# Optimization experiments

Hardware: AMD Instinct MI355X
Metric: run time of the kernel (lower is better)

## Reference

```python
import jax, jax.numpy as jnp
import numpy as np
from jax import lax

B, H, W, C = 8, 128, 128, 256
HEADS, DHEAD = 8, 32
INNER = HEADS * DHEAD  # == C, required by pos_emb reshape


def setup_inputs() -> dict:
    key = jax.random.key(0)
    ks = jax.random.split(key, 12)
    s = 0.02
    return {
        "x_in": jax.random.normal(ks[0], (B, H, W, C), jnp.float32),
        "Wq": jax.random.normal(ks[1], (INNER, C), jnp.float32) * s,
        "Wk": jax.random.normal(ks[2], (INNER, C), jnp.float32) * s,
        "Wv": jax.random.normal(ks[3], (INNER, C), jnp.float32) * s,
        "rescale": jnp.ones((HEADS, 1, 1), jnp.float32),
        "Wp": jax.random.normal(ks[4], (C, INNER), jnp.float32) * s,
        "bp": jnp.zeros((C,), jnp.float32),
        "Wc1": jax.random.normal(ks[5], (INNER, INNER, 3, 3), jnp.float32) * s,
        "bc1": jnp.zeros((INNER,), jnp.float32),
        "Wc2": jax.random.normal(ks[6], (INNER, INNER, 3, 3), jnp.float32) * s,
        "bc2": jnp.zeros((INNER,), jnp.float32),
    }


def _l2norm(x, axis=-1, eps=1e-12):
    n = jnp.sqrt(jnp.sum(x * x, axis=axis, keepdims=True))
    return x / jnp.maximum(n, eps)


def _conv(x, w, b):
    y = lax.conv_general_dilated(x, w, (1, 1), 'SAME',
                                 dimension_numbers=('NCHW', 'OIHW', 'NCHW'))
    return y + b[None, :, None, None]


def reference(x_in, Wq, Wk, Wv, rescale, Wp, bp, Wc1, bc1, Wc2, bc2):
    b, h, w, c = x_in.shape
    n = h * w
    x = x_in.reshape(b, n, c)
    q_inp = x @ Wq.T  # [b, n, inner]
    k_inp = x @ Wk.T
    v_inp = x @ Wv.T

    def heads(t):  # b n (h d) -> b h d n  (already transposed)
        return t.reshape(b, n, HEADS, DHEAD).transpose(0, 2, 3, 1)

    q = _l2norm(heads(q_inp))  # [b, heads, d, n], normalized over n
    k = _l2norm(heads(k_inp))
    v = heads(v_inp)  # [b, heads, d, n]

    attn = jnp.einsum('bhdn,bhen->bhde', k, q) * rescale  # [b, heads, d, d]
    attn = jax.nn.softmax(attn, axis=-1)
    xo = jnp.einsum('bhde,bhen->bhdn', attn, v)  # [b, heads, d, n]
    xo = xo.transpose(0, 3, 1, 2).reshape(b, n, INNER)  # b n (heads d)
    out_c = (xo @ Wp.T + bp).reshape(b, h, w, c)

    vp = v_inp.reshape(b, h, w, INNER).transpose(0, 3, 1, 2)  # NCHW
    p = _conv(vp, Wc1, bc1)
    p = jax.nn.gelu(p, approximate=False)
    p = _conv(p, Wc2, bc2)
    out_p = p.transpose(0, 2, 3, 1)  # b h w c
    return out_c, out_p
```

## Files before the change

### kernel.cpp

```cpp
#include <hip/hip_runtime.h>
#include <cstdint>

#define DEV __device__ __forceinline__

typedef __bf16 bf16x8 __attribute__((ext_vector_type(8)));
typedef float f32x4 __attribute__((ext_vector_type(4)));
typedef unsigned int u32;
typedef unsigned short u16;

DEV u16 f2bf(float f) {
  u32 u = __builtin_bit_cast(u32, f);
  u += 0x7fffu + ((u >> 16) & 1u);
  return (u16)(u >> 16);
}
DEV float bf2f(u16 b) { return __builtin_bit_cast(float, (u32)b << 16); }

DEV void gload16(const u16* g, u16* l) {
  __builtin_amdgcn_global_load_lds(
      (const __attribute__((address_space(1))) u32*)g,
      (__attribute__((address_space(3))) u32*)(uintptr_t)l, 16, 0, 0);
}

DEV void border_body(u16* __restrict__ p, int idx) {
  int pix = idx >> 5, c8 = (idx & 31) << 3;
  int b = pix / 516, r = pix % 516;
  int x, y;
  if (r < 130)      { y = 0;   x = r; }
  else if (r < 260) { y = 129; x = r - 130; }
  else if (r < 388) { x = 0;   y = r - 259; }
  else              { x = 129; y = r - 387; }
  u16* dst = p + (((long)b * 130 + y) * 130 + x) * 256 + c8;
  *reinterpret_cast<uint4*>(dst) = uint4{0, 0, 0, 0};
}

__global__ void cvt_f32_bf16(const float* __restrict__ in, u16* __restrict__ out, int n4) {
  int i = blockIdx.x * blockDim.x + threadIdx.x;
  if (i >= n4) return;
  float4 v = reinterpret_cast<const float4*>(in)[i];
  ushort4 o;
  o.x = f2bf(v.x); o.y = f2bf(v.y); o.z = f2bf(v.z); o.w = f2bf(v.w);
  reinterpret_cast<ushort4*>(out)[i] = o;
}

__global__ void prep(const float* __restrict__ Wq, const float* __restrict__ Wk,
                     const float* __restrict__ Wv, const float* __restrict__ Wc1,
                     const float* __restrict__ Wc2, u16* __restrict__ wqkv,
                     u16* __restrict__ wc1r, u16* __restrict__ wc2r, u16* __restrict__ vpad) {
  const int blk = blockIdx.x, t = threadIdx.x;
  if (blk < 192) {
    const float* src = blk < 64 ? Wq : (blk < 128 ? Wk : Wv);
    u16* dst = wqkv + (blk < 64 ? 0 : (blk < 128 ? 65536 : 131072));
    const int i = (blk & 63) * 256 + t;
    float4 v = reinterpret_cast<const float4*>(src)[i];
    ushort4 o;
    o.x = f2bf(v.x); o.y = f2bf(v.y); o.z = f2bf(v.z); o.w = f2bf(v.w);
    reinterpret_cast<ushort4*>(dst)[i] = o;
  } else if (blk < 4800) {
    const int q = blk - 192;
    const float* w = q < 2304 ? Wc1 : Wc2;
    u16* dst = q < 2304 ? wc1r : wc2r;
    const int j = (q % 2304) * 256 + t;
    const int oc = j / 2304, r = j - oc * 2304;
    const int kt = r >> 6, c_lo = r & 63;
    const int cg = kt / 9, slab = kt - cg * 9;
    const int ic = cg * 64 + c_lo;
    dst[j] = f2bf(w[(oc * 256 + ic) * 9 + slab]);
  } else {
    const int idx = (blk - 4800) * 256 + t;
    if (idx < 8 * 516 * 32) border_body(vpad, idx);
  }
}

template <int CONV, int KTOT, int EPI, int PERB, int SWZ>
__global__ __launch_bounds__(512, 1) void mm8(
    const u16* __restrict__ A, const u16* __restrict__ Bt,
    const float* __restrict__ bias, void* __restrict__ out,
    u16* __restrict__ vp) {
  extern __shared__ u16 lds[];
  constexpr int NKT = KTOT / 64;
  constexpr int NITER = NKT / 2;
  const int tid = threadIdx.x;
  const int wave = tid >> 6, lane = tid & 63;
  const int wr = wave >> 2, wcid = wave & 3;
  const int lrow = lane & 15, lk = lane >> 4;
  int bid = (int)blockIdx.x;
  int tile, colbase;
  if (SWZ == 1) {
    const int xcd = bid & 7, k = bid >> 3;
    tile = (xcd + ((k >> 5) << 3)) * 32 + (k & 31);
    colbase = 0;
  } else if (SWZ == 2) {
    const int xcd = bid & 7, s = bid >> 3;
    const int r = s / 3;
    tile = xcd * 64 + r;
    colbase = (s - r * 3) * 256;
  } else {
    tile = (bid & 7) * 64 + (bid >> 3);
    colbase = 0;
  }
  const long rowbase = (long)tile * 256;
  const int bimg = tile >> 6;
  const int y0 = (tile & 63) * 2;
  const u16* BT = PERB ? Bt + (long)bimg * 65536 : Bt;

  auto STAGE = [&](int kt, int isB, int half, int bufq) {
#pragma unroll
    for (int j = 0; j < 2; ++j) {
      const int idx = j * 512 + tid;
      const int rh = idx >> 3;
      const int sg = (idx & 7) ^ (rh & 7);
      const u16* g;
      if (isB) {
        g = BT + (long)(colbase + half * 128 + rh) * KTOT + kt * 64 + sg * 8;
      } else if (CONV == 1) {
        const int cg = kt / 9;
        const int slab = kt - cg * 9;
        const int ky = slab / 3 - 1, kx = slab - (slab / 3) * 3 - 1;
        const int c0 = cg * 64;
        g = A + (((long)bimg * 130 + (y0 + half) + 1 + ky) * 130 + (rh + 1 + kx)) * 256 + c0 + sg * 8;
      } else if (CONV == 2) {
        g = A + (((long)bimg * 130 + (y0 + half) + 1) * 130 + (rh + 1)) * 256 + kt * 64 + sg * 8;
      } else {
        g = A + (rowbase + half * 128 + rh) * (long)256 + kt * 64 + sg * 8;
      }
      u16* l = lds + (isB ? 32768 : 0) + bufq * 16384 + half * 8192 + (j * 512 + wave * 64) * 8;
      gload16(g, l);
    }
  };

  f32x4 acc[8][4] = {};
  bf16x8 bq[4][2];

  STAGE(0, 1, 0, 0); STAGE(0, 1, 1, 0);
  STAGE(0, 0, 0, 0); STAGE(0, 0, 1, 0);
  STAGE(1, 1, 0, 1); STAGE(1, 1, 1, 1);
  asm volatile("s_waitcnt vmcnt(4)" ::: "memory");
  __builtin_amdgcn_s_barrier();
  __builtin_amdgcn_sched_barrier(0);

  for (int it = 0; it < NITER; ++it) {
    const int u0 = 2 * it;
#pragma unroll
    for (int ph = 0; ph < 8; ++ph) {
      constexpr int S_ISB[8]  = {0, 0, 1, 1, 0, 0, 1, 1};
      constexpr int S_HALF[8] = {0, 1, 0, 1, 0, 1, 0, 1};
      constexpr int S_BUF[8]  = {1, 1, 0, 0, 0, 0, 1, 1};
      constexpr int S_DT[8]   = {1, 1, 2, 2, 2, 2, 3, 3};
      const int cbuf = ph >> 2, quad = ph & 3;
      if (quad == 0) {
#pragma unroll
        for (int nf = 0; nf < 4; ++nf)
#pragma unroll
          for (int ks = 0; ks < 2; ++ks) {
            const int n = wcid * 64 + nf * 16 + lrow;
            const int slot = (ks * 4 + lk) ^ (n & 7);
            bq[nf][ks] = *reinterpret_cast<const bf16x8*>(&lds[32768 + cbuf * 16384 + n * 64 + slot * 8]);
          }
      }
      bf16x8 aq[2][2];
#pragma unroll
      for (int mf = 0; mf < 2; ++mf)
#pragma unroll
        for (int ks = 0; ks < 2; ++ks) {
          const int r = wr * 128 + quad * 32 + mf * 16 + lrow;
          const int slot = (ks * 4 + lk) ^ (r & 7);
          aq[mf][ks] = *reinterpret_cast<const bf16x8*>(&lds[cbuf * 16384 + r * 64 + slot * 8]);
        }
      int st = u0 + S_DT[ph];
      if (st > NKT - 1) st = NKT - 1;
      STAGE(st, S_ISB[ph], S_HALF[ph], S_BUF[ph]);
      if (quad == 0)
        asm volatile("s_waitcnt lgkmcnt(8)" ::: "memory");
      __builtin_amdgcn_s_barrier();
      asm volatile("s_waitcnt lgkmcnt(0)" ::: "memory");
      __builtin_amdgcn_sched_barrier(0);
      __builtin_amdgcn_s_setprio(1);
#pragma unroll
      for (int mf = 0; mf < 2; ++mf)
#pragma unroll
        for (int nf = 0; nf < 4; ++nf)
#pragma unroll
          for (int ks = 0; ks < 2; ++ks)
            acc[quad * 2 + mf][nf] = __builtin_amdgcn_mfma_f32_16x16x32_bf16(
                aq[mf][ks], bq[nf][ks], acc[quad * 2 + mf][nf], 0, 0, 0);
      __builtin_amdgcn_s_setprio(0);
      __builtin_amdgcn_sched_barrier(0);
      if (quad == 3)
        asm volatile("s_waitcnt vmcnt(4)" ::: "memory");
      __builtin_amdgcn_s_barrier();
      __builtin_amdgcn_sched_barrier(0);
    }
  }

  const int r0 = (lane >> 4) * 4;
  const int occ = lane & 15;
#pragma unroll
  for (int M = 0; M < 8; ++M) {
#pragma unroll
    for (int nf = 0; nf < 4; ++nf) {
      const int col = wcid * 64 + nf * 16 + occ;
      const int col4 = col & ~3;
#pragma unroll
      for (int i = 0; i < 4; ++i) {
        const int p = wr * 128 + M * 16 + r0 + i;
        float v = acc[M][nf][i];
        if (EPI == 1) {
          v += bias[col];
          float s1 = __shfl_xor(v, 1);
          float s2 = __shfl_xor(v, 2);
          float s3 = __shfl_xor(s1, 2);
          if ((lane & 3) == 0)
            *reinterpret_cast<float4*>(reinterpret_cast<float*>(out) + (rowbase + p) * 256 + col4) =
                float4{v, s1, s2, s3};
        } else {
          if (EPI == 2) {
            v += bias[col];
            v = 0.5f * v * (1.0f + erff(v * 0.70710678118654752f));
          }
          u32 me = f2bf(v);
          u32 n1 = (u32)__shfl_xor((int)me, 1);
          u32 pair = (lane & 1) ? ((me << 16) | n1) : (me | (n1 << 16));
          u32 p2 = (u32)__shfl_xor((int)pair, 2);
          if ((lane & 3) == 0) {
            if (EPI == 2) {
              const int y = y0 + (p >> 7), x = p & 127;
              *reinterpret_cast<uint2*>(reinterpret_cast<u16*>(out) +
                  (((long)bimg * 130 + y + 1) * 130 + x + 1) * 256 + col4) = uint2{pair, p2};
            } else {
              const int gcol4 = colbase + col4;
              const long rowpix = rowbase + p;
              if (gcol4 < 512) {
                *reinterpret_cast<uint2*>(reinterpret_cast<u16*>(out) + rowpix * 512 + gcol4) =
                    uint2{pair, p2};
              } else {
                const int b_ = (int)(rowpix >> 14), rem = (int)(rowpix & 16383);
                *reinterpret_cast<uint2*>(vp + (((long)b_ * 130 + (rem >> 7) + 1) * 130 +
                    (rem & 127) + 1) * 256 + (gcol4 - 512)) = uint2{pair, p2};
              }
            }
          }
        }
      }
    }
  }
}

__global__ __launch_bounds__(256) void gram_mfma(const u16* __restrict__ qkv,
                                                 float* __restrict__ G,
                                                 float* __restrict__ norm2) {
  __shared__ __align__(16) u16 kT[2][32][40];
  __shared__ __align__(16) u16 qT[2][32][40];
  __shared__ float redq[256][4];
  __shared__ float redk[256][4];
  const int nc = blockIdx.x;
  const int bh = blockIdx.y;
  const int b = bh >> 3, h = bh & 7;
  const int t = threadIdx.x;
  const int wave = t >> 6, lane = t & 63;
  const int mh = wave >> 1, nh = wave & 1;
  const int r = t >> 3, cg = (t & 7) * 4;
  const long n0 = (long)b * 16384 + (long)nc * 4096;
  const u16* qp = qkv + n0 * 512 + h * 32;
  const u16* kp = qp + 256;
  f32x4 acc = {0.f, 0.f, 0.f, 0.f};
  float sq[4] = {0, 0, 0, 0}, sk[4] = {0, 0, 0, 0};

  ushort4 pq[4], pk[4];
#pragma unroll
  for (int j = 0; j < 4; ++j) {
    pq[j] = *reinterpret_cast<const ushort4*>(qp + (long)(j * 32 + r) * 512 + cg);
    pk[j] = *reinterpret_cast<const ushort4*>(kp + (long)(j * 32 + r) * 512 + cg);
  }

  for (int s4 = 0; s4 < 32; ++s4) {
#pragma unroll
    for (int c = 0; c < 4; ++c) {
      const int s = s4 * 4 + c;
      const int buf = s & 1;
      kT[buf][cg + 0][r] = pk[c].x; kT[buf][cg + 1][r] = pk[c].y;
      kT[buf][cg + 2][r] = pk[c].z; kT[buf][cg + 3][r] = pk[c].w;
      qT[buf][cg + 0][r] = pq[c].x; qT[buf][cg + 1][r] = pq[c].y;
      qT[buf][cg + 2][r] = pq[c].z; qT[buf][cg + 3][r] = pq[c].w;
      float f;
      f = bf2f(pq[c].x); sq[0] += f * f;
      f = bf2f(pq[c].y); sq[1] += f * f;
      f = bf2f(pq[c].z); sq[2] += f * f;
      f = bf2f(pq[c].w); sq[3] += f * f;
      f = bf2f(pk[c].x); sk[0] += f * f;
      f = bf2f(pk[c].y); sk[1] += f * f;
      f = bf2f(pk[c].z); sk[2] += f * f;
      f = bf2f(pk[c].w); sk[3] += f * f;
      if (s + 4 < 128) {
        pq[c] = *reinterpret_cast<const ushort4*>(qp + (long)((s + 4) * 32 + r) * 512 + cg);
        pk[c] = *reinterpret_cast<const ushort4*>(kp + (long)((s + 4) * 32 + r) * 512 + cg);
      }
      __syncthreads();
      bf16x8 af = *reinterpret_cast<const bf16x8*>(&kT[buf][mh * 16 + (lane & 15)][(lane >> 4) * 8]);
      bf16x8 bf = *reinterpret_cast<const bf16x8*>(&qT[buf][nh * 16 + (lane & 15)][(lane >> 4) * 8]);
      acc = __builtin_amdgcn_mfma_f32_16x16x32_bf16(af, bf, acc, 0, 0, 0);
    }
  }

  float* gp = G + (long)bh * 1024 + (mh * 16 + (lane >> 4) * 4) * 32 + nh * 16 + (lane & 15);
#pragma unroll
  for (int i = 0; i < 4; ++i) atomicAdd(gp + i * 32, acc[i]);

  __syncthreads();
#pragma unroll
  for (int j = 0; j < 4; ++j) { redq[t][j] = sq[j]; redk[t][j] = sk[j]; }
  __syncthreads();
  if (t < 64) {
    const int qk = t >> 5;
    const int colid = t & 31;
    const int cgi = colid >> 2, j = colid & 3;
    float s = 0.f;
#pragma unroll
    for (int r2 = 0; r2 < 32; ++r2)
      s += qk ? redk[r2 * 8 + cgi][j] : redq[r2 * 8 + cgi][j];
    atomicAdd(&norm2[b * 512 + qk * 256 + h * 32 + colid], s);
  }
}

__global__ void attn_softmax(const float* __restrict__ G, const float* __restrict__ norm2,
                             const float* __restrict__ rescale, float* __restrict__ attn) {
  const int bh = blockIdx.x;
  const int b = bh >> 3, h = bh & 7;
  const int t = threadIdx.x;
  __shared__ float iqs[32], iks[32];
  if (t < 32) {
    iqs[t] = 1.0f / fmaxf(sqrtf(norm2[b * 512 + h * 32 + t]), 1e-12f);
    iks[t] = 1.0f / fmaxf(sqrtf(norm2[b * 512 + 256 + h * 32 + t]), 1e-12f);
  }
  __syncthreads();
  if (t < 32) {
    const float rs = rescale[h];
    const float ikd = iks[t] * rs;
    const float* gp = G + ((long)bh * 32 + t) * 32;
    float l[32];
    float mx = -1e30f;
#pragma unroll
    for (int e = 0; e < 32; ++e) {
      l[e] = gp[e] * ikd * iqs[e];
      mx = fmaxf(mx, l[e]);
    }
    float s = 0.f;
#pragma unroll
    for (int e = 0; e < 32; ++e) {
      l[e] = expf(l[e] - mx);
      s += l[e];
    }
    const float inv = 1.0f / s;
    float* op = attn + ((long)bh * 32 + t) * 32;
#pragma unroll
    for (int e = 0; e < 32; ++e) op[e] = l[e] * inv;
  }
}

__global__ __launch_bounds__(256) void weff_border(const float* __restrict__ Wp,
                                                   const float* __restrict__ attn,
                                                   u16* __restrict__ weff,
                                                   u16* __restrict__ p1pad) {
  const int blk = blockIdx.x;
  const int t = threadIdx.x;
  if (blk < 64) {
    __shared__ float A[32][33];
    const int b = blk >> 3, h = blk & 7;
    const float* ap = attn + (long)blk * 1024;
    for (int j = t; j < 1024; j += 256) A[j >> 5][j & 31] = ap[j];
    __syncthreads();
    const float* wrow = Wp + (long)t * 256 + h * 32;
    float w[32];
#pragma unroll
    for (int d = 0; d < 32; ++d) w[d] = wrow[d];
    u16* orow = weff + ((long)b * 256 + t) * 256 + h * 32;
#pragma unroll
    for (int e = 0; e < 32; ++e) {
      float s = 0.f;
#pragma unroll
      for (int d = 0; d < 32; ++d) s += w[d] * A[d][e];
      orow[e] = f2bf(s);
    }
  } else {
    const int idx = (blk - 64) * 256 + t;
    if (idx < 8 * 516 * 32) border_body(p1pad, idx);
  }
}

extern "C" void kernel_launch(void* const* d_in, const int* in_sizes, int n_in,
                              void* d_out, int out_size, void* d_ws, size_t ws_size,
                              hipStream_t stream) {
  const float* x = (const float*)d_in[0];
  const float* Wq = (const float*)d_in[1];
  const float* Wk = (const float*)d_in[2];
  const float* Wv = (const float*)d_in[3];
  const float* resc = (const float*)d_in[4];
  const float* Wp = (const float*)d_in[5];
  const float* bp = (const float*)d_in[6];
  const float* Wc1 = (const float*)d_in[7];
  const float* bc1 = (const float*)d_in[8];
  const float* Wc2 = (const float*)d_in[9];
  const float* bc2 = (const float*)d_in[10];

  char* ws = (char*)d_ws;
  u16* qkv   = (u16*)(ws + 0L);
  u16* p1pad = (u16*)(ws + 0L);
  u16* vpad  = (u16*)(ws + 134217728L);
  u16* xb    = (u16*)(ws + 203440128L);
  u16* wqkv  = (u16*)(ws + 270548992L);
  u16* wc1r  = (u16*)(ws + 270942208L);
  u16* wc2r  = (u16*)(ws + 272121856L);
  u16* weff  = (u16*)(ws + 273301504L);
  float* norm2 = (float*)(ws + 274350080L);
  float* G     = (float*)(ws + 274366464L);
  float* attn  = (float*)(ws + 274628608L);

  float* out_c = (float*)d_out;
  float* out_p = out_c + 33554432L;

  hipMemsetAsync(norm2, 0, 16384 + 262144, stream);

  cvt_f32_bf16<<<32768, 256, 0, stream>>>(x, xb, 8388608);
  prep<<<5316, 256, 0, stream>>>(Wq, Wk, Wv, Wc1, Wc2, wqkv, wc1r, wc2r, vpad);

  mm8<0, 256, 0, 0, 2><<<1536, 512, 131072, stream>>>(xb, wqkv, nullptr, qkv, vpad);

  gram_mfma<<<dim3(4, 64), 256, 0, stream>>>(qkv, G, norm2);
  attn_softmax<<<64, 64, 0, stream>>>(G, norm2, resc, attn);
  weff_border<<<580, 256, 0, stream>>>(Wp, attn, weff, p1pad);

  mm8<2, 256, 1, 1, 0><<<512, 512, 131072, stream>>>(vpad, weff, bp, out_c, nullptr);

  mm8<1, 2304, 2, 0, 1><<<512, 512, 131072, stream>>>(vpad, wc1r, bc1, p1pad, nullptr);
  mm8<1, 2304, 1, 0, 1><<<512, 512, 131072, stream>>>(p1pad, wc2r, bc2, out_p, nullptr);
}
```

Before: 629.2 us.

## Precompute per-lane load base pointers and use scalar epilogue stores

The staging lambda now computes per-lane global base pointers once, outside the loop. Each stage only adds a uniform int offset, which should cut per-iteration VALU address arithmetic in the pipelined GEMM loop. The epilogue drops the shuffle-based packing into float4/uint2 vector stores and has each lane write its own scalar element. This removes cross-lane shuffles but issues four times as many narrow, strided global stores, and the 32-bit uofs arithmetic could overflow for large offsets.

```diff
diff --git a/kernel.cpp b/kernel.cpp
--- a/kernel.cpp
+++ b/kernel.cpp
@@ -103,29 +103,31 @@
   const int y0 = (tile & 63) * 2;
   const u16* BT = PERB ? Bt + (long)bimg * 65536 : Bt;
 
+  const int rh0 = tid >> 3;
+  const int sg0 = (tid & 7) ^ (rh0 & 7);
+  const u16* laneA0 = A + rh0 * 256 + sg0 * 8;
+  const u16* laneA1 = laneA0 + 64 * 256;
+  const u16* laneB0 = BT + (long)rh0 * KTOT + sg0 * 8;
+  const u16* laneB1 = laneB0 + (long)64 * KTOT;
+  u16* ldsl = lds + wave * 512;
+
   auto STAGE = [&](int kt, int isB, int half, int bufq) {
-#pragma unroll
-    for (int j = 0; j < 2; ++j) {
-      const int idx = j * 512 + tid;
-      const int rh = idx >> 3;
-      const int sg = (idx & 7) ^ (rh & 7);
-      const u16* g;
-      if (isB) {
-        g = BT + (long)(colbase + half * 128 + rh) * KTOT + kt * 64 + sg * 8;
-      } else if (CONV == 1) {
-        const int cg = kt / 9;
-        const int slab = kt - cg * 9;
-        const int ky = slab / 3 - 1, kx = slab - (slab / 3) * 3 - 1;
-        const int c0 = cg * 64;
-        g = A + (((long)bimg * 130 + (y0 + half) + 1 + ky) * 130 + (rh + 1 + kx)) * 256 + c0 + sg * 8;
-      } else if (CONV == 2) {
-        g = A + (((long)bimg * 130 + (y0 + half) + 1) * 130 + (rh + 1)) * 256 + kt * 64 + sg * 8;
-      } else {
-        g = A + (rowbase + half * 128 + rh) * (long)256 + kt * 64 + sg * 8;
-      }
-      u16* l = lds + (isB ? 32768 : 0) + bufq * 16384 + half * 8192 + (j * 512 + wave * 64) * 8;
-      gload16(g, l);
-    }
+    int uofs;
+    if (isB) {
+      uofs = (colbase + half * 128) * KTOT + kt * 64;
+    } else if (CONV == 1) {
+      const int cg = kt / 9;
+      const int slab = kt - cg * 9;
+      const int ky = slab / 3 - 1, kx = slab - (slab / 3) * 3 - 1;
+      uofs = ((bimg * 130 + y0 + half + 1 + ky) * 130 + 1 + kx) * 256 + cg * 64;
+    } else if (CONV == 2) {
+      uofs = ((bimg * 130 + y0 + half + 1) * 130 + 1) * 256 + kt * 64;
+    } else {
+      uofs = (int)(rowbase + half * 128) * 256 + kt * 64;
+    }
+    u16* l = ldsl + (isB ? 32768 : 0) + bufq * 16384 + half * 8192;
+    gload16((isB ? laneB0 : laneA0) + uofs, l);
+    gload16((isB ? laneB1 : laneA1) + uofs, l + 4096);
   };
 
   f32x4 acc[8][4] = {};
@@ -199,46 +201,26 @@
 #pragma unroll
     for (int nf = 0; nf < 4; ++nf) {
       const int col = wcid * 64 + nf * 16 + occ;
-      const int col4 = col & ~3;
 #pragma unroll
       for (int i = 0; i < 4; ++i) {
         const int p = wr * 128 + M * 16 + r0 + i;
         float v = acc[M][nf][i];
-        if (EPI == 1) {
+        if (EPI == 0) {
+          const long rowpix = rowbase + p;
+          const int gcol = colbase + col;
+          if (gcol < 512) {
+            reinterpret_cast<u16*>(out)[rowpix * 512 + gcol] = f2bf(v);
+          } else {
+            const int b = (int)(rowpix >> 14), rem = (int)(rowpix & 16383);
+            vp[(((long)b * 130 + (rem >> 7) + 1) * 130 + (rem & 127) + 1) * 256 + (gcol - 512)] = f2bf(v);
+          }
+        } else if (EPI == 1) {
+          reinterpret_cast<float*>(out)[(rowbase + p) * 256 + col] = v + bias[col];
+        } else {
           v += bias[col];
-          float s1 = __shfl_xor(v, 1);
-          float s2 = __shfl_xor(v, 2);
-          float s3 = __shfl_xor(s1, 2);
-          if ((lane & 3) == 0)
-            *reinterpret_cast<float4*>(reinterpret_cast<float*>(out) + (rowbase + p) * 256 + col4) =
-                float4{v, s1, s2, s3};
-        } else {
-          if (EPI == 2) {
-            v += bias[col];
-            v = 0.5f * v * (1.0f + erff(v * 0.70710678118654752f));
-          }
-          u32 me = f2bf(v);
-          u32 n1 = (u32)__shfl_xor((int)me, 1);
-          u32 pair = (lane & 1) ? ((me << 16) | n1) : (me | (n1 << 16));
-          u32 p2 = (u32)__shfl_xor((int)pair, 2);
-          if ((lane & 3) == 0) {
-            if (EPI == 2) {
-              const int y = y0 + (p >> 7), x = p & 127;
-              *reinterpret_cast<uint2*>(reinterpret_cast<u16*>(out) +
-                  (((long)bimg * 130 + y + 1) * 130 + x + 1) * 256 + col4) = uint2{pair, p2};
-            } else {
-              const int gcol4 = colbase + col4;
-              const long rowpix = rowbase + p;
-              if (gcol4 < 512) {
-                *reinterpret_cast<uint2*>(reinterpret_cast<u16*>(out) + rowpix * 512 + gcol4) =
-                    uint2{pair, p2};
-              } else {
-                const int b_ = (int)(rowpix >> 14), rem = (int)(rowpix & 16383);
-                *reinterpret_cast<uint2*>(vp + (((long)b_ * 130 + (rem >> 7) + 1) * 130 +
-                    (rem & 127) + 1) * 256 + (gcol4 - 512)) = uint2{pair, p2};
-              }
-            }
-          }
+          v = 0.5f * v * (1.0f + erff(v * 0.70710678118654752f));
+          const int y = y0 + (p >> 7), x = p & 127;
+          reinterpret_cast<u16*>(out)[(((long)bimg * 130 + y + 1) * 130 + x + 1) * 256 + col] = f2bf(v);
         }
       }
     }
```

Result: faster. 556.3 us, median of 2 (-11.6%).
